# Kernel tuning notes

Measured on AMD Instinct MI355X. Metric: run time of the kernel, lower is better.

## Reference

```python
import jax, jax.numpy as jnp
import numpy as np

N = 50000      # nodes
E = 800000     # edges (before self loops)
IN = 128       # in_channels
H = 8          # heads
C = 32         # hidden_channels per head
HC = H * C     # 256, concat head dim
G = 256        # number of graphs
NEG_SLOPE = 0.2  # PyG GATConv default


def gat_conv(h_in, src, dst, W, att_s, att_d, bias):
    """PyG-style GATConv, concat heads. src/dst include self loops.
    h_in: [N, F_in]; W: [H*C, F_in]; att_s/att_d: [H, C]; bias: [H*C]."""
    h = (h_in @ W.T).reshape(N, H, C)                      # [N,H,C]
    a_s = jnp.sum(h * att_s, axis=-1)                      # [N,H]
    a_d = jnp.sum(h * att_d, axis=-1)                      # [N,H]
    e = jax.nn.leaky_relu(a_s[src] + a_d[dst], NEG_SLOPE)  # [E',H]
    # segment softmax over incoming edges of each dst node
    m = jax.ops.segment_max(e, dst, num_segments=N)        # [N,H]
    p = jnp.exp(e - m[dst])                                # [E',H]
    denom = jax.ops.segment_sum(p, dst, num_segments=N)    # [N,H]
    alpha = p / denom[dst]                                 # [E',H]
    msg = alpha[:, :, None] * h[src]                       # [E',H,C]
    out = jax.ops.segment_sum(msg, dst, num_segments=N)    # [N,H,C]
    return out.reshape(N, HC) + bias


def setup_inputs() -> dict:
    key = jax.random.key(0)
    ks = jax.random.split(key, 20)
    s = 0.1
    inp = {
        "x": jax.random.normal(ks[0], (N, IN), jnp.float32),
        "edge_index": jax.random.randint(ks[1], (2, E), 0, N, dtype=jnp.int64),
        "batch": jnp.sort(jax.random.randint(ks[2], (N,), 0, G, dtype=jnp.int64)),
        # layer 1: IN -> H*C
        "W1": jax.random.normal(ks[3], (HC, IN), jnp.float32) * s,
        "as1": jax.random.normal(ks[4], (H, C), jnp.float32) * s,
        "ad1": jax.random.normal(ks[5], (H, C), jnp.float32) * s,
        "b1": jnp.zeros((HC,), jnp.float32),
        # layer 2: H*C -> H*C
        "W2": jax.random.normal(ks[6], (HC, HC), jnp.float32) * s,
        "as2": jax.random.normal(ks[7], (H, C), jnp.float32) * s,
        "ad2": jax.random.normal(ks[8], (H, C), jnp.float32) * s,
        "b2": jnp.zeros((HC,), jnp.float32),
        # layer 3: H*C -> H*C
        "W3": jax.random.normal(ks[9], (HC, HC), jnp.float32) * s,
        "as3": jax.random.normal(ks[10], (H, C), jnp.float32) * s,
        "ad3": jax.random.normal(ks[11], (H, C), jnp.float32) * s,
        "b3": jnp.zeros((HC,), jnp.float32),
        # final linear H*C -> 1
        "Wf": jax.random.normal(ks[12], (1, HC), jnp.float32) * s,
        "bf": jnp.zeros((1,), jnp.float32),
    }
    return inp


def reference(x, edge_index, batch, W1, as1, ad1, b1, W2, as2, ad2, b2,
              W3, as3, ad3, b3, Wf, bf):
    # add self loops once (PyG GATConv default add_self_loops=True)
    loop = jnp.arange(N, dtype=edge_index.dtype)
    src = jnp.concatenate([edge_index[0], loop])
    dst = jnp.concatenate([edge_index[1], loop])

    h = jax.nn.relu(gat_conv(x, src, dst, W1, as1, ad1, b1))
    # dropout p=0.01, eval mode -> identity
    h = jax.nn.relu(gat_conv(h, src, dst, W2, as2, ad2, b2))
    h = gat_conv(h, src, dst, W3, as3, ad3, b3)

    # global mean pool per graph
    sums = jax.ops.segment_sum(h, batch, num_segments=G)          # [G,HC]
    cnt = jax.ops.segment_sum(jnp.ones((N, 1), h.dtype), batch, num_segments=G)
    pooled = sums / jnp.maximum(cnt, 1.0)                         # [G,HC]
    return pooled @ Wf.T + bf                                     # [G,1]
```

## Files before the change

kernel.cpp:

```cpp
#include <hip/hip_runtime.h>

#define N_NODES 50000
#define E_EDGES 800000
#define E_EXT   850000
#define IN_CH   128
#define HC      256
#define NHEAD   8
#define CH      32
#define NGRAPH  256
#define SCAN_CHUNK 1024
#define N_CHUNKS ((N_NODES + SCAN_CHUNK - 1) / SCAN_CHUNK)

typedef __bf16 bf16x8 __attribute__((ext_vector_type(8)));
typedef float  f32x4  __attribute__((ext_vector_type(4)));

__device__ inline ushort f2bf(float f) {
    union { float f; unsigned u; } v; v.f = f;
    unsigned u = v.u;
    unsigned r = u + 0x7FFFu + ((u >> 16) & 1u);
    return (ushort)(r >> 16);
}
__device__ inline float bflo(unsigned u) {
    union { unsigned u; float f; } v; v.u = u << 16; return v.f;
}
__device__ inline float bfhi(unsigned u) {
    union { unsigned u; float f; } v; v.u = u & 0xFFFF0000u; return v.f;
}

__global__ __launch_bounds__(256) void cvt_bf16_kernel(
    const float* __restrict__ in, ushort* __restrict__ outp, int n4)
{
    int i = blockIdx.x * blockDim.x + threadIdx.x;
    if (i >= n4) return;
    float4 v = *(const float4*)(in + (size_t)i * 4);
    ushort4 o;
    o.x = f2bf(v.x); o.y = f2bf(v.y); o.z = f2bf(v.z); o.w = f2bf(v.w);
    *(ushort4*)(outp + (size_t)i * 4) = o;
}

#define W1_N4 (HC * IN_CH / 4)
#define W23_N4 (HC * HC / 4)
__global__ __launch_bounds__(256) void cvt_weights_kernel(
    const float* __restrict__ W1, const float* __restrict__ W2,
    const float* __restrict__ W3,
    ushort* __restrict__ W1b, ushort* __restrict__ W2b, ushort* __restrict__ W3b)
{
    int i = blockIdx.x * blockDim.x + threadIdx.x;
    const float* src; ushort* dst; int k;
    if (i < W1_N4) { src = W1; dst = W1b; k = i; }
    else if (i < W1_N4 + W23_N4) { src = W2; dst = W2b; k = i - W1_N4; }
    else if (i < W1_N4 + 2 * W23_N4) { src = W3; dst = W3b; k = i - W1_N4 - W23_N4; }
    else return;
    float4 v = *(const float4*)(src + (size_t)k * 4);
    ushort4 o;
    o.x = f2bf(v.x); o.y = f2bf(v.y); o.z = f2bf(v.z); o.w = f2bf(v.w);
    *(ushort4*)(dst + (size_t)k * 4) = o;
}

__global__ __launch_bounds__(256) void mfma_gemm_kernel(
    const ushort* __restrict__ Xb, const ushort* __restrict__ Wb,
    ushort* __restrict__ Hb, int M, int F)
{
    __shared__ ushort As[128][40];
    __shared__ ushort Bs[128][40];
    const int tid  = threadIdx.x;
    const int lane = tid & 63;
    const int wave = tid >> 6;
    const int wr = (wave >> 1) * 64;
    const int wc = (wave & 1) * 64;
    const int bm = blockIdx.x * 128;
    const int bn = blockIdx.y * 128;
    const int lrow = tid >> 2;
    const int lseg = (tid & 3) * 8;
    const int fr = lane & 15;
    const int fk = (lane >> 4) * 8;

    f32x4 zero = {0.f, 0.f, 0.f, 0.f};
    f32x4 acc[4][4];
    #pragma unroll
    for (int i = 0; i < 4; i++)
        #pragma unroll
        for (int j = 0; j < 4; j++) acc[i][j] = zero;

    for (int k0 = 0; k0 < F; k0 += 32) {
        #pragma unroll
        for (int rr = 0; rr < 2; rr++) {
            int row = lrow + rr * 64;
            int arow = bm + row;
            bf16x8 av = {};
            if (arow < M) av = *(const bf16x8*)(Xb + (size_t)arow * F + k0 + lseg);
            *(bf16x8*)(&As[row][lseg]) = av;
            bf16x8 bv = *(const bf16x8*)(Wb + (size_t)(bn + row) * F + k0 + lseg);
            *(bf16x8*)(&Bs[row][lseg]) = bv;
        }
        __syncthreads();
        bf16x8 a[4], b[4];
        #pragma unroll
        for (int i = 0; i < 4; i++) {
            a[i] = *(const bf16x8*)(&As[wr + i * 16 + fr][fk]);
            b[i] = *(const bf16x8*)(&Bs[wc + i * 16 + fr][fk]);
        }
        #pragma unroll
        for (int i = 0; i < 4; i++)
            #pragma unroll
            for (int j = 0; j < 4; j++)
                acc[i][j] = __builtin_amdgcn_mfma_f32_16x16x32_bf16(
                    a[i], b[j], acc[i][j], 0, 0, 0);
        __syncthreads();
    }
    const int rb = (lane >> 4) * 4;
    #pragma unroll
    for (int i = 0; i < 4; i++) {
        #pragma unroll
        for (int r = 0; r < 4; r++) {
            int m = bm + wr + i * 16 + rb + r;
            if (m < M) {
                #pragma unroll
                for (int j = 0; j < 4; j++)
                    Hb[(size_t)m * HC + bn + wc + j * 16 + fr] = f2bf(acc[i][j][r]);
            }
        }
    }
}

__global__ __launch_bounds__(256) void att_kernel(
    const ushort* __restrict__ hb,
    const float* __restrict__ att_s, const float* __restrict__ att_d,
    float* __restrict__ a_s, float* __restrict__ a_d)
{
    int idx = blockIdx.x * blockDim.x + threadIdx.x;
    if (idx >= N_NODES * NHEAD) return;
    int n = idx >> 3, hh = idx & 7;
    const uint4* row = (const uint4*)(hb + (size_t)n * HC + hh * CH);
    const float4* vs = (const float4*)(att_s + hh * CH);
    const float4* vd = (const float4*)(att_d + hh * CH);
    float ss = 0.f, sd = 0.f;
    #pragma unroll
    for (int q = 0; q < 4; q++) {
        uint4 u = row[q];
        float h0 = bflo(u.x), h1 = bfhi(u.x), h2 = bflo(u.y), h3 = bfhi(u.y);
        float h4 = bflo(u.z), h5 = bfhi(u.z), h6 = bflo(u.w), h7 = bfhi(u.w);
        float4 s0 = vs[q * 2], s1 = vs[q * 2 + 1];
        float4 d0 = vd[q * 2], d1 = vd[q * 2 + 1];
        ss += h0 * s0.x + h1 * s0.y + h2 * s0.z + h3 * s0.w
            + h4 * s1.x + h5 * s1.y + h6 * s1.z + h7 * s1.w;
        sd += h0 * d0.x + h1 * d0.y + h2 * d0.z + h3 * d0.w
            + h4 * d1.x + h5 * d1.y + h6 * d1.z + h7 * d1.w;
    }
    a_s[idx] = ss; a_d[idx] = sd;
}

__global__ __launch_bounds__(256) void att3_kernel(
    const ushort* __restrict__ hb,
    const float* __restrict__ att_s, const float* __restrict__ att_d,
    const float* __restrict__ Wf, const float* __restrict__ b3,
    float2* __restrict__ q, float* __restrict__ a_d, float* __restrict__ bw)
{
    int idx = blockIdx.x * blockDim.x + threadIdx.x;
    if (blockIdx.x == 0 && threadIdx.x < NHEAD) {
        float s = 0.f;
        for (int c = 0; c < CH; c++)
            s += b3[threadIdx.x * CH + c] * Wf[threadIdx.x * CH + c];
        bw[threadIdx.x] = s;
    }
    if (idx >= N_NODES * NHEAD) return;
    int n = idx >> 3, hh = idx & 7;
    const uint4* row = (const uint4*)(hb + (size_t)n * HC + hh * CH);
    const float4* vs = (const float4*)(att_s + hh * CH);
    const float4* vd = (const float4*)(att_d + hh * CH);
    const float4* vw = (const float4*)(Wf + hh * CH);
    float ss = 0.f, sd = 0.f, sw = 0.f;
    #pragma unroll
    for (int qq = 0; qq < 4; qq++) {
        uint4 u = row[qq];
        float h0 = bflo(u.x), h1 = bfhi(u.x), h2 = bflo(u.y), h3 = bfhi(u.y);
        float h4 = bflo(u.z), h5 = bfhi(u.z), h6 = bflo(u.w), h7 = bfhi(u.w);
        float4 s0 = vs[qq * 2], s1 = vs[qq * 2 + 1];
        float4 d0 = vd[qq * 2], d1 = vd[qq * 2 + 1];
        float4 w0 = vw[qq * 2], w1 = vw[qq * 2 + 1];
        ss += h0 * s0.x + h1 * s0.y + h2 * s0.z + h3 * s0.w
            + h4 * s1.x + h5 * s1.y + h6 * s1.z + h7 * s1.w;
        sd += h0 * d0.x + h1 * d0.y + h2 * d0.z + h3 * d0.w
            + h4 * d1.x + h5 * d1.y + h6 * d1.z + h7 * d1.w;
        sw += h0 * w0.x + h1 * w0.y + h2 * w0.z + h3 * w0.w
            + h4 * w1.x + h5 * w1.y + h6 * w1.z + h7 * w1.w;
    }
    q[idx] = make_float2(ss, sw);
    a_d[idx] = sd;
}

__global__ __launch_bounds__(256) void hist_kernel(
    const int* __restrict__ ei, int* __restrict__ deg)
{
    int eid = blockIdx.x * blockDim.x + threadIdx.x;
    if (eid >= E_EXT) return;
    int d = (eid < E_EDGES) ? ei[E_EDGES + eid] : (eid - E_EDGES);
    atomicAdd(&deg[d], 1);
}

__global__ void scan1_kernel(const int* __restrict__ deg,
                             int* __restrict__ row_ptr, int* __restrict__ csum)
{
    __shared__ int buf[SCAN_CHUNK];
    int t = threadIdx.x;
    int base = blockIdx.x * SCAN_CHUNK;
    int v = (base + t < N_NODES) ? deg[base + t] : 0;
    buf[t] = v;
    __syncthreads();
    for (int off = 1; off < SCAN_CHUNK; off <<= 1) {
        int x = buf[t];
        int y = (t >= off) ? buf[t - off] : 0;
        __syncthreads();
        buf[t] = x + y;
        __syncthreads();
    }
    if (base + t < N_NODES) row_ptr[base + t] = buf[t] - v;
    if (t == SCAN_CHUNK - 1) csum[blockIdx.x] = buf[t];
}

__global__ void scan2_kernel(int* __restrict__ csum)
{
    __shared__ int buf[64];
    int t = threadIdx.x;
    int v = (t < N_CHUNKS) ? csum[t] : 0;
    buf[t] = v;
    __syncthreads();
    for (int off = 1; off < 64; off <<= 1) {
        int x = buf[t];
        int y = (t >= off) ? buf[t - off] : 0;
        __syncthreads();
        buf[t] = x + y;
        __syncthreads();
    }
    if (t < N_CHUNKS) csum[t] = buf[t] - v;
}

__global__ void scan3_kernel(int* __restrict__ row_ptr, const int* __restrict__ csum)
{
    int i = blockIdx.x * blockDim.x + threadIdx.x;
    if (i < N_NODES) row_ptr[i] += csum[i / SCAN_CHUNK];
    if (i == 0) row_ptr[N_NODES] = E_EXT;
}

__global__ __launch_bounds__(256) void scatter_kernel(
    const int* __restrict__ ei, const int* __restrict__ row_ptr,
    int* __restrict__ cur, int* __restrict__ esrc)
{
    int eid = blockIdx.x * blockDim.x + threadIdx.x;
    if (eid >= E_EXT) return;
    int s, d;
    if (eid < E_EDGES) { s = ei[eid]; d = ei[E_EDGES + eid]; }
    else { s = eid - E_EDGES; d = s; }
    int pos = row_ptr[d] + atomicAdd(&cur[d], 1);
    esrc[pos] = s;
}

__global__ __launch_bounds__(256) void gather_kernel(
    const int* __restrict__ row_ptr, const int* __restrict__ esrc,
    const ushort* __restrict__ hb,
    const float* __restrict__ a_s, const float* __restrict__ a_d,
    const float* __restrict__ bias,
    ushort* __restrict__ out_b)
{
    int wv = (blockIdx.x * blockDim.x + threadIdx.x) >> 6;
    int lane = threadIdx.x & 63;
    int half = lane >> 5;
    int lloc = lane & 31;
    int n = wv * 2 + half;
    if (n >= N_NODES) return;
    const int hh = lloc >> 2;
    const int shbase = half << 5;
    const float adv = a_d[n * NHEAD + hh];
    const int beg = row_ptr[n], end = row_ptr[n + 1];

    float a0=0.f,a1=0.f,a2=0.f,a3=0.f,a4=0.f,a5=0.f,a6=0.f,a7=0.f,den=0.f;

    for (int base = beg; base < end; base += 32) {
        int cnt = min(32, end - base);
        int sv = (base + lloc < end) ? esrc[base + lloc] : 0;
        int j = 0;
        for (; j + 4 <= cnt; j += 4) {
            int s0 = __shfl(sv, shbase + j);
            int s1 = __shfl(sv, shbase + j + 1);
            int s2 = __shfl(sv, shbase + j + 2);
            int s3 = __shfl(sv, shbase + j + 3);
            float e0 = a_s[s0 * NHEAD + hh];
            float e1 = a_s[s1 * NHEAD + hh];
            float e2 = a_s[s2 * NHEAD + hh];
            float e3 = a_s[s3 * NHEAD + hh];
            uint4 u0 = *(const uint4*)(hb + (size_t)s0 * HC + lloc * 8);
            uint4 u1 = *(const uint4*)(hb + (size_t)s1 * HC + lloc * 8);
            uint4 u2 = *(const uint4*)(hb + (size_t)s2 * HC + lloc * 8);
            uint4 u3 = *(const uint4*)(hb + (size_t)s3 * HC + lloc * 8);
            e0 += adv; e0 = (e0 > 0.f) ? e0 : 0.2f * e0; float w0 = __expf(e0);
            e1 += adv; e1 = (e1 > 0.f) ? e1 : 0.2f * e1; float w1 = __expf(e1);
            e2 += adv; e2 = (e2 > 0.f) ? e2 : 0.2f * e2; float w2 = __expf(e2);
            e3 += adv; e3 = (e3 > 0.f) ? e3 : 0.2f * e3; float w3 = __expf(e3);
            den += (w0 + w1) + (w2 + w3);
            a0 = fmaf(w0, bflo(u0.x), a0); a1 = fmaf(w0, bfhi(u0.x), a1);
            a2 = fmaf(w0, bflo(u0.y), a2); a3 = fmaf(w0, bfhi(u0.y), a3);
            a4 = fmaf(w0, bflo(u0.z), a4); a5 = fmaf(w0, bfhi(u0.z), a5);
            a6 = fmaf(w0, bflo(u0.w), a6); a7 = fmaf(w0, bfhi(u0.w), a7);
            a0 = fmaf(w1, bflo(u1.x), a0); a1 = fmaf(w1, bfhi(u1.x), a1);
            a2 = fmaf(w1, bflo(u1.y), a2); a3 = fmaf(w1, bfhi(u1.y), a3);
            a4 = fmaf(w1, bflo(u1.z), a4); a5 = fmaf(w1, bfhi(u1.z), a5);
            a6 = fmaf(w1, bflo(u1.w), a6); a7 = fmaf(w1, bfhi(u1.w), a7);
            a0 = fmaf(w2, bflo(u2.x), a0); a1 = fmaf(w2, bfhi(u2.x), a1);
            a2 = fmaf(w2, bflo(u2.y), a2); a3 = fmaf(w2, bfhi(u2.y), a3);
            a4 = fmaf(w2, bflo(u2.z), a4); a5 = fmaf(w2, bfhi(u2.z), a5);
            a6 = fmaf(w2, bflo(u2.w), a6); a7 = fmaf(w2, bfhi(u2.w), a7);
            a0 = fmaf(w3, bflo(u3.x), a0); a1 = fmaf(w3, bfhi(u3.x), a1);
            a2 = fmaf(w3, bflo(u3.y), a2); a3 = fmaf(w3, bfhi(u3.y), a3);
            a4 = fmaf(w3, bflo(u3.z), a4); a5 = fmaf(w3, bfhi(u3.z), a5);
            a6 = fmaf(w3, bflo(u3.w), a6); a7 = fmaf(w3, bfhi(u3.w), a7);
        }
        for (; j < cnt; j++) {
            int s = __shfl(sv, shbase + j);
            float e = a_s[s * NHEAD + hh] + adv;
            e = (e > 0.f) ? e : 0.2f * e;
            float w = __expf(e);
            den += w;
            uint4 u = *(const uint4*)(hb + (size_t)s * HC + lloc * 8);
            a0 = fmaf(w, bflo(u.x), a0); a1 = fmaf(w, bfhi(u.x), a1);
            a2 = fmaf(w, bflo(u.y), a2); a3 = fmaf(w, bfhi(u.y), a3);
            a4 = fmaf(w, bflo(u.z), a4); a5 = fmaf(w, bfhi(u.z), a5);
            a6 = fmaf(w, bflo(u.w), a6); a7 = fmaf(w, bfhi(u.w), a7);
        }
    }
    float inv = 1.f / den;
    float4 ba = *(const float4*)(bias + lloc * 8);
    float4 bb = *(const float4*)(bias + lloc * 8 + 4);
    float o0 = fmaf(a0, inv, ba.x), o1 = fmaf(a1, inv, ba.y);
    float o2 = fmaf(a2, inv, ba.z), o3 = fmaf(a3, inv, ba.w);
    float o4 = fmaf(a4, inv, bb.x), o5 = fmaf(a5, inv, bb.y);
    float o6 = fmaf(a6, inv, bb.z), o7 = fmaf(a7, inv, bb.w);
    o0 = fmaxf(o0, 0.f); o1 = fmaxf(o1, 0.f); o2 = fmaxf(o2, 0.f); o3 = fmaxf(o3, 0.f);
    o4 = fmaxf(o4, 0.f); o5 = fmaxf(o5, 0.f); o6 = fmaxf(o6, 0.f); o7 = fmaxf(o7, 0.f);
    uint4 ob;
    ob.x = (unsigned)f2bf(o0) | ((unsigned)f2bf(o1) << 16);
    ob.y = (unsigned)f2bf(o2) | ((unsigned)f2bf(o3) << 16);
    ob.z = (unsigned)f2bf(o4) | ((unsigned)f2bf(o5) << 16);
    ob.w = (unsigned)f2bf(o6) | ((unsigned)f2bf(o7) << 16);
    *(uint4*)(out_b + (size_t)n * HC + lloc * 8) = ob;
}

__global__ __launch_bounds__(256) void light_gather_kernel(
    const int* __restrict__ row_ptr, const int* __restrict__ esrc,
    const float2* __restrict__ q, const float* __restrict__ a_d,
    const float* __restrict__ bw, float* __restrict__ ndot)
{
    int idx = blockIdx.x * blockDim.x + threadIdx.x;
    if (idx >= N_NODES * NHEAD) return;
    int n = idx >> 3, hh = idx & 7;
    const float adv = a_d[idx];
    const int beg = row_ptr[n], end = row_ptr[n + 1];
    float acc = 0.f, den = 0.f;
    int e = beg;
    for (; e + 4 <= end; e += 4) {
        int s0 = esrc[e], s1 = esrc[e + 1], s2 = esrc[e + 2], s3 = esrc[e + 3];
        float2 q0 = q[s0 * NHEAD + hh];
        float2 q1 = q[s1 * NHEAD + hh];
        float2 q2 = q[s2 * NHEAD + hh];
        float2 q3 = q[s3 * NHEAD + hh];
        float t0 = q0.x + adv; t0 = (t0 > 0.f) ? t0 : 0.2f * t0; float w0 = __expf(t0);
        float t1 = q1.x + adv; t1 = (t1 > 0.f) ? t1 : 0.2f * t1; float w1 = __expf(t1);
        float t2 = q2.x + adv; t2 = (t2 > 0.f) ? t2 : 0.2f * t2; float w2 = __expf(t2);
        float t3 = q3.x + adv; t3 = (t3 > 0.f) ? t3 : 0.2f * t3; float w3 = __expf(t3);
        den += (w0 + w1) + (w2 + w3);
        acc = fmaf(w0, q0.y, acc); acc = fmaf(w1, q1.y, acc);
        acc = fmaf(w2, q2.y, acc); acc = fmaf(w3, q3.y, acc);
    }
    for (; e < end; e++) {
        int s = esrc[e];
        float2 qv = q[s * NHEAD + hh];
        float t = qv.x + adv; t = (t > 0.f) ? t : 0.2f * t;
        float w = __expf(t);
        den += w;
        acc = fmaf(w, qv.y, acc);
    }
    float p = acc / den + bw[hh];
    #pragma unroll
    for (int off = 4; off > 0; off >>= 1) p += __shfl_xor(p, off);
    if (hh == 0) ndot[n] = p;
}

__global__ __launch_bounds__(256) void pool2_kernel(
    const float* __restrict__ ndot, const int* __restrict__ batch,
    const float* __restrict__ bf, float* __restrict__ outp)
{
    __shared__ float red[256];
    int g = blockIdx.x, t = threadIdx.x;
    int lo = 0, hi = N_NODES;
    while (lo < hi) { int mid = (lo + hi) >> 1; if (batch[mid] < g) lo = mid + 1; else hi = mid; }
    int start = lo;
    lo = 0; hi = N_NODES;
    while (lo < hi) { int mid = (lo + hi) >> 1; if (batch[mid] < g + 1) lo = mid + 1; else hi = mid; }
    int end = lo;
    float s = 0.f;
    for (int i = start + t; i < end; i += 256) s += ndot[i];
    red[t] = s;
    __syncthreads();
    for (int k = 128; k > 0; k >>= 1) {
        if (t < k) red[t] += red[t + k];
        __syncthreads();
    }
    if (t == 0) outp[g] = red[0] / fmaxf((float)(end - start), 1.f) + bf[0];
}

extern "C" void kernel_launch(void* const* d_in, const int* in_sizes, int n_in,
                              void* d_out, int out_size, void* d_ws, size_t ws_size,
                              hipStream_t stream)
{
    const float* x    = (const float*)d_in[0];
    const int*   ei   = (const int*)d_in[1];
    const int*   batch= (const int*)d_in[2];
    const float* W1   = (const float*)d_in[3];
    const float* as1  = (const float*)d_in[4];
    const float* ad1  = (const float*)d_in[5];
    const float* b1   = (const float*)d_in[6];
    const float* W2   = (const float*)d_in[7];
    const float* as2  = (const float*)d_in[8];
    const float* ad2  = (const float*)d_in[9];
    const float* b2   = (const float*)d_in[10];
    const float* W3   = (const float*)d_in[11];
    const float* as3  = (const float*)d_in[12];
    const float* ad3  = (const float*)d_in[13];
    const float* b3   = (const float*)d_in[14];
    const float* Wf   = (const float*)d_in[15];
    const float* bf   = (const float*)d_in[16];
    float* out = (float*)d_out;

    char* ws = (char*)d_ws;
    size_t off = 0;
    auto allocb = [&](size_t bytes) {
        void* p = ws + off;
        off += (bytes + 255) & ~(size_t)255;
        return p;
    };
    ushort* bufA    = (ushort*)allocb((size_t)N_NODES * HC * 2);
    ushort* bufB    = (ushort*)allocb((size_t)N_NODES * HC * 2);
    ushort* W1b     = (ushort*)allocb((size_t)HC * IN_CH * 2);
    ushort* W2b     = (ushort*)allocb((size_t)HC * HC * 2);
    ushort* W3b     = (ushort*)allocb((size_t)HC * HC * 2);
    float*  as_buf  = (float*) allocb((size_t)N_NODES * NHEAD * 4);
    float*  ad_buf  = (float*) allocb((size_t)N_NODES * NHEAD * 4);
    float2* q_buf   = (float2*)allocb((size_t)N_NODES * NHEAD * 8);
    float*  bw_buf  = (float*) allocb(NHEAD * 4);
    int*    deg     = (int*)   allocb(N_NODES * 4);
    int*    cur     = (int*)   allocb(N_NODES * 4);
    int*    row_ptr = (int*)   allocb((N_NODES + 1) * 4);
    int*    csum    = (int*)   allocb(64 * 4);
    int*    esrc    = (int*)   allocb(E_EXT * 4);
    float*  ndot    = (float*) allocb(N_NODES * 4);
    (void)ws_size; (void)in_sizes; (void)n_in; (void)out_size;

    cvt_bf16_kernel<<<((size_t)N_NODES * IN_CH / 4 + 255) / 256, 256, 0, stream>>>(
        x, bufA, N_NODES * IN_CH / 4);
    cvt_weights_kernel<<<(W1_N4 + 2 * W23_N4 + 255) / 256, 256, 0, stream>>>(
        W1, W2, W3, W1b, W2b, W3b);

    hipMemsetAsync(deg, 0, N_NODES * sizeof(int), stream);
    hipMemsetAsync(cur, 0, N_NODES * sizeof(int), stream);
    hist_kernel<<<(E_EXT + 255) / 256, 256, 0, stream>>>(ei, deg);
    scan1_kernel<<<N_CHUNKS, SCAN_CHUNK, 0, stream>>>(deg, row_ptr, csum);
    scan2_kernel<<<1, 64, 0, stream>>>(csum);
    scan3_kernel<<<(N_NODES + 255) / 256, 256, 0, stream>>>(row_ptr, csum);
    scatter_kernel<<<(E_EXT + 255) / 256, 256, 0, stream>>>(ei, row_ptr, cur, esrc);

    dim3 ggrid((N_NODES + 127) / 128, HC / 128);
    const int gather_blocks = (((N_NODES + 1) / 2) * 64 + 255) / 256;
    const int att_blocks = (N_NODES * NHEAD + 255) / 256;

    mfma_gemm_kernel<<<ggrid, 256, 0, stream>>>(bufA, W1b, bufB, N_NODES, IN_CH);
    att_kernel<<<att_blocks, 256, 0, stream>>>(bufB, as1, ad1, as_buf, ad_buf);
    gather_kernel<<<gather_blocks, 256, 0, stream>>>(
        row_ptr, esrc, bufB, as_buf, ad_buf, b1, bufA);
    mfma_gemm_kernel<<<ggrid, 256, 0, stream>>>(bufA, W2b, bufB, N_NODES, HC);
    att_kernel<<<att_blocks, 256, 0, stream>>>(bufB, as2, ad2, as_buf, ad_buf);
    gather_kernel<<<gather_blocks, 256, 0, stream>>>(
        row_ptr, esrc, bufB, as_buf, ad_buf, b2, bufA);
    mfma_gemm_kernel<<<ggrid, 256, 0, stream>>>(bufA, W3b, bufB, N_NODES, HC);
    att3_kernel<<<att_blocks, 256, 0, stream>>>(
        bufB, as3, ad3, Wf, b3, q_buf, ad_buf, bw_buf);
    light_gather_kernel<<<att_blocks, 256, 0, stream>>>(
        row_ptr, esrc, q_buf, ad_buf, bw_buf, ndot);

    pool2_kernel<<<NGRAPH, 256, 0, stream>>>(ndot, batch, bf, out);
}
```

Measured before the change: 370.1 us.

## Fuse attention-score dot products and input bf16 conversion into GEMM epilogue

Computes the per-head source/destination attention scores (and the final-layer Wf projection) directly from the fp32 MFMA accumulators in the GEMM epilogue, using cross-lane shuffles, and removes the separate att/att3 kernels. The first-layer GEMM now reads fp32 x and converts it to bf16 while loading, which removes the standalone conversion kernel. The layer-3 GEMM no longer writes its H output at all, since only the scalar projections are needed. This saves several full passes over the N×256 feature buffer and a few launches. In exchange the epilogue does extra shuffle work, and the scores now come from unrounded fp32 values instead of the bf16-rounded H.

```diff
diff --git a/kernel.cpp b/kernel.cpp
--- a/kernel.cpp
+++ b/kernel.cpp
@@ -27,17 +27,6 @@
     union { unsigned u; float f; } v; v.u = u & 0xFFFF0000u; return v.f;
 }
 
-__global__ __launch_bounds__(256) void cvt_bf16_kernel(
-    const float* __restrict__ in, ushort* __restrict__ outp, int n4)
-{
-    int i = blockIdx.x * blockDim.x + threadIdx.x;
-    if (i >= n4) return;
-    float4 v = *(const float4*)(in + (size_t)i * 4);
-    ushort4 o;
-    o.x = f2bf(v.x); o.y = f2bf(v.y); o.z = f2bf(v.z); o.w = f2bf(v.w);
-    *(ushort4*)(outp + (size_t)i * 4) = o;
-}
-
 #define W1_N4 (HC * IN_CH / 4)
 #define W23_N4 (HC * HC / 4)
 __global__ __launch_bounds__(256) void cvt_weights_kernel(
@@ -57,9 +46,24 @@
     *(ushort4*)(dst + (size_t)k * 4) = o;
 }
 
+__global__ void bw_kernel(const float* __restrict__ b3, const float* __restrict__ Wf,
+                          float* __restrict__ bw)
+{
+    int h = threadIdx.x;
+    if (h >= NHEAD) return;
+    float s = 0.f;
+    for (int c = 0; c < CH; c++) s += b3[h * CH + c] * Wf[h * CH + c];
+    bw[h] = s;
+}
+
 __global__ __launch_bounds__(256) void mfma_gemm_kernel(
-    const ushort* __restrict__ Xb, const ushort* __restrict__ Wb,
-    ushort* __restrict__ Hb, int M, int F)
+    const ushort* __restrict__ Xb, const float* __restrict__ Xf,
+    const ushort* __restrict__ Wb,
+    ushort* __restrict__ Hb, int M, int F,
+    const float* __restrict__ att_s, const float* __restrict__ att_d,
+    const float* __restrict__ wf,
+    float* __restrict__ as_out, float* __restrict__ ad_out,
+    float2* __restrict__ q_out)
 {
     __shared__ ushort As[128][40];
     __shared__ ushort Bs[128][40];
@@ -88,7 +92,17 @@
             int row = lrow + rr * 64;
             int arow = bm + row;
             bf16x8 av = {};
-            if (arow < M) av = *(const bf16x8*)(Xb + (size_t)arow * F + k0 + lseg);
+            if (Xf) {
+                if (arow < M) {
+                    float4 lo = *(const float4*)(Xf + (size_t)arow * F + k0 + lseg);
+                    float4 hi = *(const float4*)(Xf + (size_t)arow * F + k0 + lseg + 4);
+                    ushort t[8] = { f2bf(lo.x), f2bf(lo.y), f2bf(lo.z), f2bf(lo.w),
+                                    f2bf(hi.x), f2bf(hi.y), f2bf(hi.z), f2bf(hi.w) };
+                    av = *(const bf16x8*)t;
+                }
+            } else {
+                if (arow < M) av = *(const bf16x8*)(Xb + (size_t)arow * F + k0 + lseg);
+            }
             *(bf16x8*)(&As[row][lseg]) = av;
             bf16x8 bv = *(const bf16x8*)(Wb + (size_t)(bn + row) * F + k0 + lseg);
             *(bf16x8*)(&Bs[row][lseg]) = bv;
@@ -108,85 +122,60 @@
                     a[i], b[j], acc[i][j], 0, 0, 0);
         __syncthreads();
     }
+
     const int rb = (lane >> 4) * 4;
+    const int h0 = (bn >> 5) + (wc >> 5);
+
+    const float wsa0 = att_s[h0 * CH + fr],        wsa1 = att_s[h0 * CH + 16 + fr];
+    const float wda0 = att_d[h0 * CH + fr],        wda1 = att_d[h0 * CH + 16 + fr];
+    const float wsb0 = att_s[(h0 + 1) * CH + fr],  wsb1 = att_s[(h0 + 1) * CH + 16 + fr];
+    const float wdb0 = att_d[(h0 + 1) * CH + fr],  wdb1 = att_d[(h0 + 1) * CH + 16 + fr];
+    float wfa0 = 0.f, wfa1 = 0.f, wfb0 = 0.f, wfb1 = 0.f;
+    if (wf) {
+        wfa0 = wf[h0 * CH + fr];       wfa1 = wf[h0 * CH + 16 + fr];
+        wfb0 = wf[(h0 + 1) * CH + fr]; wfb1 = wf[(h0 + 1) * CH + 16 + fr];
+    }
+
     #pragma unroll
     for (int i = 0; i < 4; i++) {
         #pragma unroll
         for (int r = 0; r < 4; r++) {
             int m = bm + wr + i * 16 + rb + r;
-            if (m < M) {
+            if (Hb && m < M) {
                 #pragma unroll
                 for (int j = 0; j < 4; j++)
                     Hb[(size_t)m * HC + bn + wc + j * 16 + fr] = f2bf(acc[i][j][r]);
             }
+            float psa = acc[i][0][r] * wsa0 + acc[i][1][r] * wsa1;
+            float pda = acc[i][0][r] * wda0 + acc[i][1][r] * wda1;
+            float psb = acc[i][2][r] * wsb0 + acc[i][3][r] * wsb1;
+            float pdb = acc[i][2][r] * wdb0 + acc[i][3][r] * wdb1;
+            float pwa = 0.f, pwb = 0.f;
+            if (wf) {
+                pwa = acc[i][0][r] * wfa0 + acc[i][1][r] * wfa1;
+                pwb = acc[i][2][r] * wfb0 + acc[i][3][r] * wfb1;
+            }
+            #pragma unroll
+            for (int off = 1; off < 16; off <<= 1) {
+                psa += __shfl_xor(psa, off);
+                pda += __shfl_xor(pda, off);
+                psb += __shfl_xor(psb, off);
+                pdb += __shfl_xor(pdb, off);
+                if (wf) { pwa += __shfl_xor(pwa, off); pwb += __shfl_xor(pwb, off); }
+            }
+            if (fr == 0 && m < M) {
+                if (q_out) {
+                    q_out[m * NHEAD + h0]     = make_float2(psa, pwa);
+                    q_out[m * NHEAD + h0 + 1] = make_float2(psb, pwb);
+                } else {
+                    as_out[m * NHEAD + h0]     = psa;
+                    as_out[m * NHEAD + h0 + 1] = psb;
+                }
+                ad_out[m * NHEAD + h0]     = pda;
+                ad_out[m * NHEAD + h0 + 1] = pdb;
+            }
         }
     }
-}
-
-__global__ __launch_bounds__(256) void att_kernel(
-    const ushort* __restrict__ hb,
-    const float* __restrict__ att_s, const float* __restrict__ att_d,
-    float* __restrict__ a_s, float* __restrict__ a_d)
-{
-    int idx = blockIdx.x * blockDim.x + threadIdx.x;
-    if (idx >= N_NODES * NHEAD) return;
-    int n = idx >> 3, hh = idx & 7;
-    const uint4* row = (const uint4*)(hb + (size_t)n * HC + hh * CH);
-    const float4* vs = (const float4*)(att_s + hh * CH);
-    const float4* vd = (const float4*)(att_d + hh * CH);
-    float ss = 0.f, sd = 0.f;
-    #pragma unroll
-    for (int q = 0; q < 4; q++) {
-        uint4 u = row[q];
-        float h0 = bflo(u.x), h1 = bfhi(u.x), h2 = bflo(u.y), h3 = bfhi(u.y);
-        float h4 = bflo(u.z), h5 = bfhi(u.z), h6 = bflo(u.w), h7 = bfhi(u.w);
-        float4 s0 = vs[q * 2], s1 = vs[q * 2 + 1];
-        float4 d0 = vd[q * 2], d1 = vd[q * 2 + 1];
-        ss += h0 * s0.x + h1 * s0.y + h2 * s0.z + h3 * s0.w
-            + h4 * s1.x + h5 * s1.y + h6 * s1.z + h7 * s1.w;
-        sd += h0 * d0.x + h1 * d0.y + h2 * d0.z + h3 * d0.w
-            + h4 * d1.x + h5 * d1.y + h6 * d1.z + h7 * d1.w;
-    }
-    a_s[idx] = ss; a_d[idx] = sd;
-}
-
-__global__ __launch_bounds__(256) void att3_kernel(
-    const ushort* __restrict__ hb,
-    const float* __restrict__ att_s, const float* __restrict__ att_d,
-    const float* __restrict__ Wf, const float* __restrict__ b3,
-    float2* __restrict__ q, float* __restrict__ a_d, float* __restrict__ bw)
-{
-    int idx = blockIdx.x * blockDim.x + threadIdx.x;
-    if (blockIdx.x == 0 && threadIdx.x < NHEAD) {
-        float s = 0.f;
-        for (int c = 0; c < CH; c++)
-            s += b3[threadIdx.x * CH + c] * Wf[threadIdx.x * CH + c];
-        bw[threadIdx.x] = s;
-    }
-    if (idx >= N_NODES * NHEAD) return;
-    int n = idx >> 3, hh = idx & 7;
-    const uint4* row = (const uint4*)(hb + (size_t)n * HC + hh * CH);
-    const float4* vs = (const float4*)(att_s + hh * CH);
-    const float4* vd = (const float4*)(att_d + hh * CH);
-    const float4* vw = (const float4*)(Wf + hh * CH);
-    float ss = 0.f, sd = 0.f, sw = 0.f;
-    #pragma unroll
-    for (int qq = 0; qq < 4; qq++) {
-        uint4 u = row[qq];
-        float h0 = bflo(u.x), h1 = bfhi(u.x), h2 = bflo(u.y), h3 = bfhi(u.y);
-        float h4 = bflo(u.z), h5 = bfhi(u.z), h6 = bflo(u.w), h7 = bfhi(u.w);
-        float4 s0 = vs[qq * 2], s1 = vs[qq * 2 + 1];
-        float4 d0 = vd[qq * 2], d1 = vd[qq * 2 + 1];
-        float4 w0 = vw[qq * 2], w1 = vw[qq * 2 + 1];
-        ss += h0 * s0.x + h1 * s0.y + h2 * s0.z + h3 * s0.w
-            + h4 * s1.x + h5 * s1.y + h6 * s1.z + h7 * s1.w;
-        sd += h0 * d0.x + h1 * d0.y + h2 * d0.z + h3 * d0.w
-            + h4 * d1.x + h5 * d1.y + h6 * d1.z + h7 * d1.w;
-        sw += h0 * w0.x + h1 * w0.y + h2 * w0.z + h3 * w0.w
-            + h4 * w1.x + h5 * w1.y + h6 * w1.z + h7 * w1.w;
-    }
-    q[idx] = make_float2(ss, sw);
-    a_d[idx] = sd;
 }
 
 __global__ __launch_bounds__(256) void hist_kernel(
@@ -454,10 +443,9 @@
     float*  ndot    = (float*) allocb(N_NODES * 4);
     (void)ws_size; (void)in_sizes; (void)n_in; (void)out_size;
 
-    cvt_bf16_kernel<<<((size_t)N_NODES * IN_CH / 4 + 255) / 256, 256, 0, stream>>>(
-        x, bufA, N_NODES * IN_CH / 4);
     cvt_weights_kernel<<<(W1_N4 + 2 * W23_N4 + 255) / 256, 256, 0, stream>>>(
         W1, W2, W3, W1b, W2b, W3b);
+    bw_kernel<<<1, 64, 0, stream>>>(b3, Wf, bw_buf);
 
     hipMemsetAsync(deg, 0, N_NODES * sizeof(int), stream);
     hipMemsetAsync(cur, 0, N_NODES * sizeof(int), stream);
@@ -469,20 +457,21 @@
 
     dim3 ggrid((N_NODES + 127) / 128, HC / 128);
     const int gather_blocks = (((N_NODES + 1) / 2) * 64 + 255) / 256;
-    const int att_blocks = (N_NODES * NHEAD + 255) / 256;
-
-    mfma_gemm_kernel<<<ggrid, 256, 0, stream>>>(bufA, W1b, bufB, N_NODES, IN_CH);
-    att_kernel<<<att_blocks, 256, 0, stream>>>(bufB, as1, ad1, as_buf, ad_buf);
+
+    mfma_gemm_kernel<<<ggrid, 256, 0, stream>>>(
+        nullptr, x, W1b, bufB, N_NODES, IN_CH, as1, ad1, nullptr,
+        as_buf, ad_buf, nullptr);
     gather_kernel<<<gather_blocks, 256, 0, stream>>>(
         row_ptr, esrc, bufB, as_buf, ad_buf, b1, bufA);
-    mfma_gemm_kernel<<<ggrid, 256, 0, stream>>>(bufA, W2b, bufB, N_NODES, HC);
-    att_kernel<<<att_blocks, 256, 0, stream>>>(bufB, as2, ad2, as_buf, ad_buf);
+    mfma_gemm_kernel<<<ggrid, 256, 0, stream>>>(
+        bufA, nullptr, W2b, bufB, N_NODES, HC, as2, ad2, nullptr,
+        as_buf, ad_buf, nullptr);
     gather_kernel<<<gather_blocks, 256, 0, stream>>>(
         row_ptr, esrc, bufB, as_buf, ad_buf, b2, bufA);
-    mfma_gemm_kernel<<<ggrid, 256, 0, stream>>>(bufA, W3b, bufB, N_NODES, HC);
-    att3_kernel<<<att_blocks, 256, 0, stream>>>(
-        bufB, as3, ad3, Wf, b3, q_buf, ad_buf, bw_buf);
-    light_gather_kernel<<<att_blocks, 256, 0, stream>>>(
+    mfma_gemm_kernel<<<ggrid, 256, 0, stream>>>(
+        bufA, nullptr, W3b, nullptr, N_NODES, HC, as3, ad3, Wf,
+        nullptr, ad_buf, q_buf);
+    light_gather_kernel<<<(N_NODES * NHEAD + 255) / 256, 256, 0, stream>>>(
         row_ptr, esrc, q_buf, ad_buf, bw_buf, ndot);
 
     pool2_kernel<<<NGRAPH, 256, 0, stream>>>(ndot, batch, bf, out);
```

After: 358.8 us. 1.03x faster.
